# Performance work log

Hardware: AMD Instinct MI355X
Metric: run time of the kernel (lower is better)

## Reference

```python
import jax, jax.numpy as jnp
import numpy as np

AGENT, WIN = 6, 7
HEADS, DIM_HEAD = 8, 32
SCALE = DIM_HEAD ** -0.5
N = AGENT * WIN * WIN  # 294 tokens per window


def _rel_pos_index():
    # static Swin-3D relative position index, computed once in numpy
    coords = np.stack(np.meshgrid(np.arange(AGENT), np.arange(WIN), np.arange(WIN), indexing='ij'))
    flat = coords.reshape(3, -1)                      # [3, N]
    rel = flat[:, :, None] - flat[:, None, :]        # [3, N, N]
    rel = rel.transpose(1, 2, 0).copy()              # [N, N, 3]
    rel[..., 0] += AGENT - 1
    rel[..., 1] += WIN - 1
    rel[..., 2] += WIN - 1
    rel[..., 0] *= (2 * WIN - 1) * (2 * WIN - 1)
    rel[..., 1] *= 2 * WIN - 1
    return jnp.asarray(rel.sum(-1))                  # [N, N] int

RPI = _rel_pos_index()


def setup_inputs() -> dict:
    key = jax.random.key(0)
    k1, k2, k3, k4 = jax.random.split(key, 4)
    dim = 256
    x = jax.random.normal(k1, (1, AGENT, 16, 16, WIN, WIN, dim), dtype=jnp.float32)
    w_qkv = jax.random.normal(k2, (3 * HEADS * DIM_HEAD, dim), dtype=jnp.float32) * 0.02
    w_out = jax.random.normal(k3, (dim, HEADS * DIM_HEAD), dtype=jnp.float32) * 0.02
    n_bias = (2 * AGENT - 1) * (2 * WIN - 1) * (2 * WIN - 1)  # 1859
    bias_table = jax.random.normal(k4, (n_bias, HEADS), dtype=jnp.float32) * 0.02
    return {"x": x, "w_qkv": w_qkv, "w_out": w_out, "bias_table": bias_table}


def reference(x, w_qkv, w_out, bias_table):
    b, l, hx, wy, w1, w2, d = x.shape
    # 'b l x y w1 w2 d -> (b x y) (l w1 w2) d'
    xw = jnp.transpose(x, (0, 2, 3, 1, 4, 5, 6)).reshape(b * hx * wy, l * w1 * w2, d)
    qkv = xw @ w_qkv.T                                # [B, N, 3*h*dh]
    q, k, v = jnp.split(qkv, 3, axis=-1)
    def heads(t):
        B, n, _ = t.shape
        return t.reshape(B, n, HEADS, DIM_HEAD).transpose(0, 2, 1, 3)  # [B, h, N, dh]
    q, k, v = heads(q) * SCALE, heads(k), heads(v)
    sim = jnp.einsum('bhid,bhjd->bhij', q, k)        # [B, h, N, N]
    bias = bias_table[RPI]                            # [N, N, h]
    sim = sim + jnp.transpose(bias, (2, 0, 1))[None]  # broadcast over B
    attn = jax.nn.softmax(sim, axis=-1)
    out = jnp.einsum('bhij,bhjd->bhid', attn, v)      # [B, h, N, dh]
    B = b * hx * wy
    out = out.transpose(0, 2, 1, 3).reshape(B, l, w1, w2, HEADS * DIM_HEAD)
    out = out @ w_out.T                               # [B, l, w1, w2, d]
    out = out.reshape(b, hx, wy, l, w1, w2, d)
    return jnp.transpose(out, (0, 3, 1, 2, 4, 5, 6))  # b l x y w1 w2 d
```

## Files before the change

### kernel.cpp

```cpp
#include <hip/hip_runtime.h>
#include <hip/hip_bf16.h>

typedef unsigned short u16;
typedef __bf16 bf16x8_t __attribute__((ext_vector_type(8)));
typedef __bf16 bf16x4_t __attribute__((ext_vector_type(4)));
typedef float fx4 __attribute__((ext_vector_type(4)));
typedef u16 u16x8_t __attribute__((ext_vector_type(8)));
typedef u16 u16x4_t __attribute__((ext_vector_type(4)));

#define SCALE_Q 0.17677669529663687f
#define PSTR 328

__device__ __forceinline__ u16 f2bu(float f) {
  __bf16 h = (__bf16)f;
  return __builtin_bit_cast(u16, h);
}

#define GLD16(gp, lp) __builtin_amdgcn_global_load_lds( \
    (const __attribute__((address_space(1))) void*)(gp), \
    (__attribute__((address_space(3))) void*)(lp), 16, 0, 0)

__global__ void prep_x(const float* __restrict__ x, u16* __restrict__ xw) {
  int t = blockIdx.x * 256 + threadIdx.x;
  int m = t >> 5, c8 = (t & 31) * 8;
  int b = m / 294, n = m % 294;
  int hx = b >> 4, wy = b & 15;
  int l = n / 49, rem = n % 49;
  int w1 = rem / 7, w2 = rem % 7;
  size_t xoff = (((((size_t)l * 16 + hx) * 16 + wy) * 7 + w1) * 7 + w2) * 256 + c8;
  const float4* src = (const float4*)(x + xoff);
  float4 v0 = src[0], v1 = src[1];
  u16x8_t o;
  o[0] = f2bu(v0.x); o[1] = f2bu(v0.y); o[2] = f2bu(v0.z); o[3] = f2bu(v0.w);
  o[4] = f2bu(v1.x); o[5] = f2bu(v1.y); o[6] = f2bu(v1.z); o[7] = f2bu(v1.w);
  *(u16x8_t*)(xw + (size_t)m * 256 + c8) = o;
}

__global__ void prep_w(const float* __restrict__ wqkv, const float* __restrict__ wout,
                       u16* __restrict__ bqkv, u16* __restrict__ bwout) {
  int t = blockIdx.x * 256 + threadIdx.x;
  if (t < 196608) {
    float v = wqkv[t];
    if (t < 65536) v *= SCALE_Q;
    bqkv[t] = f2bu(v);
  } else {
    int i = t - 196608;
    bwout[i] = f2bu(wout[i]);
  }
}

__global__ void prep_bias(const float* __restrict__ table, u16* __restrict__ bias_pre) {
  int t = blockIdx.x * 256 + threadIdx.x;
  int lane = t & 63;
  int rest = t >> 6;
  int ct = rest % 20; rest /= 20;
  int s = rest % 19; int h = rest / 19;
  int col = ct * 16 + (lane & 15);
  int rbase = s * 16 + ((lane >> 4) << 2);
  u16x4_t o;
#pragma unroll
  for (int r = 0; r < 4; ++r) {
    float v;
    if (col >= 294) {
      v = -1e30f;
    } else {
      int i = rbase + r; if (i > 293) i = 293;
      int l1 = i / 49, r1 = i % 49, a1 = r1 / 7, b1 = r1 % 7;
      int l2 = col / 49, r2 = col % 49, a2 = r2 / 7, b2 = r2 % 7;
      int idx = (l1 - l2 + 5) * 169 + (a1 - a2 + 6) * 13 + (b1 - b2 + 6);
      v = table[idx * 8 + h];
    }
    o[r] = f2bu(v);
  }
  *(u16x4_t*)(bias_pre + (size_t)t * 4) = o;
}

template <int EPI>
__global__ __launch_bounds__(256, 2) void gemm128(const u16* __restrict__ A,
                                                  const u16* __restrict__ Bw,
                                                  u16* __restrict__ Cb,
                                                  float* __restrict__ Cf) {
  __shared__ u16 sA[128 * 32];
  __shared__ u16 sB[128 * 32];
  const int tid = threadIdx.x, lane = tid & 63, wave = tid >> 6;
  const int wr = wave >> 1, wc = wave & 1;
  const int tm = blockIdx.x, tn = blockIdx.y;
  fx4 acc[4][4] = {};
#pragma unroll 1
  for (int kt = 0; kt < 8; ++kt) {
    __syncthreads();
#pragma unroll
    for (int rnd = 0; rnd < 2; ++rnd) {
      int o = rnd * 4096 + tid * 16;
      int row = o >> 6, cb = o & 63;
      const u16* gA = A + (size_t)(tm * 128 + row) * 256 + kt * 32 + (cb >> 1);
      const u16* gB = Bw + (size_t)(tn * 128 + row) * 256 + kt * 32 + (cb >> 1);
      GLD16(gA, (char*)sA + o);
      GLD16(gB, (char*)sB + o);
    }
    __syncthreads();
    bf16x8_t af[4], bfr[4];
#pragma unroll
    for (int i = 0; i < 4; ++i)
      af[i] = *(const bf16x8_t*)&sA[(wr * 64 + i * 16 + (lane & 15)) * 32 + (lane >> 4) * 8];
#pragma unroll
    for (int j = 0; j < 4; ++j)
      bfr[j] = *(const bf16x8_t*)&sB[(wc * 64 + j * 16 + (lane & 15)) * 32 + (lane >> 4) * 8];
#pragma unroll
    for (int i = 0; i < 4; ++i)
#pragma unroll
      for (int j = 0; j < 4; ++j)
        acc[i][j] = __builtin_amdgcn_mfma_f32_16x16x32_bf16(af[i], bfr[j], acc[i][j], 0, 0, 0);
  }
  const int r0 = tm * 128 + wr * 64, c0 = tn * 128 + wc * 64;
#pragma unroll
  for (int i = 0; i < 4; ++i) {
#pragma unroll
    for (int j = 0; j < 4; ++j) {
#pragma unroll
      for (int r = 0; r < 4; ++r) {
        int row = r0 + i * 16 + (lane >> 4) * 4 + r;
        int col = c0 + j * 16 + (lane & 15);
        float v = acc[i][j][r];
        if (EPI == 0) {
          Cb[(size_t)row * 768 + col] = f2bu(v);
        } else {
          int b = row / 294, n = row % 294;
          int hx = b >> 4, wy = b & 15;
          int l = n / 49, rem = n % 49, w1 = rem / 7, w2 = rem % 7;
          size_t off = (((((size_t)l * 16 + hx) * 16 + wy) * 7 + w1) * 7 + w2) * 256 + col;
          Cf[off] = v;
        }
      }
    }
  }
}

__global__ __launch_bounds__(256, 2) void attn(const u16* __restrict__ qkv,
                                               const u16* __restrict__ bias_pre,
                                               u16* __restrict__ aout) {
  __shared__ u16 VT[32 * PSTR];
  __shared__ u16 P[4][16 * PSTR];
  const int blk = blockIdx.x;
  const int b = blk >> 3, h = blk & 7;
  const int tid = threadIdx.x, lane = tid & 63, wave = tid >> 6;
  const size_t base = (size_t)b * 294 * 768;

  for (int i = tid; i < 320 * 4; i += 256) {
    int tok = i >> 2, c8 = (i & 3) * 8;
    if (tok < 294) {
      u16x8_t v = *(const u16x8_t*)(qkv + base + (size_t)tok * 768 + 512 + h * 32 + c8);
#pragma unroll
      for (int j = 0; j < 8; ++j) VT[(c8 + j) * PSTR + tok] = v[j];
    } else {
#pragma unroll
      for (int j = 0; j < 8; ++j) VT[(c8 + j) * PSTR + tok] = 0;
    }
  }
  __syncthreads();

  u16* Pw = P[wave];
  for (int s = wave; s < 19; s += 4) {
    int qr = s * 16 + (lane & 15); if (qr > 293) qr = 293;
    bf16x8_t qf = *(const bf16x8_t*)(qkv + base + (size_t)qr * 768 + h * 32 + (lane >> 4) * 8);

    fx4 acc[20];
    const u16* bp = bias_pre + ((size_t)((h * 19 + s) * 20) * 64 + lane) * 4;
#pragma unroll
    for (int t = 0; t < 20; ++t) {
      bf16x4_t bv = *(const bf16x4_t*)(bp + t * 256);
      fx4 a; a[0] = (float)bv[0]; a[1] = (float)bv[1]; a[2] = (float)bv[2]; a[3] = (float)bv[3];
      acc[t] = a;
    }
#pragma unroll
    for (int t = 0; t < 20; ++t) {
      int kr = t * 16 + (lane & 15); if (kr > 293) kr = 293;
      bf16x8_t kf = *(const bf16x8_t*)(qkv + base + (size_t)kr * 768 + 256 + h * 32 + (lane >> 4) * 8);
      acc[t] = __builtin_amdgcn_mfma_f32_16x16x32_bf16(qf, kf, acc[t], 0, 0, 0);
    }
    float m[4], sum[4];
#pragma unroll
    for (int r = 0; r < 4; ++r) {
      float mv = acc[0][r];
#pragma unroll
      for (int t = 1; t < 20; ++t) mv = fmaxf(mv, acc[t][r]);
      mv = fmaxf(mv, __shfl_xor(mv, 1));
      mv = fmaxf(mv, __shfl_xor(mv, 2));
      mv = fmaxf(mv, __shfl_xor(mv, 4));
      mv = fmaxf(mv, __shfl_xor(mv, 8));
      m[r] = mv;
    }
#pragma unroll
    for (int r = 0; r < 4; ++r) {
      float sv = 0.f;
#pragma unroll
      for (int t = 0; t < 20; ++t) {
        float e = __expf(acc[t][r] - m[r]);
        acc[t][r] = e;
        sv += e;
      }
      sv += __shfl_xor(sv, 1);
      sv += __shfl_xor(sv, 2);
      sv += __shfl_xor(sv, 4);
      sv += __shfl_xor(sv, 8);
      sum[r] = sv;
    }
    const int prow0 = (lane >> 4) * 4;
#pragma unroll
    for (int t = 0; t < 20; ++t) {
      int pc = t * 16 + (lane & 15);
#pragma unroll
      for (int r = 0; r < 4; ++r) Pw[(prow0 + r) * PSTR + pc] = f2bu(acc[t][r]);
    }
    fx4 o0 = {}, o1 = {};
#pragma unroll
    for (int kt = 0; kt < 10; ++kt) {
      bf16x8_t pf = *(const bf16x8_t*)&Pw[(lane & 15) * PSTR + kt * 32 + (lane >> 4) * 8];
      bf16x8_t v0 = *(const bf16x8_t*)&VT[(lane & 15) * PSTR + kt * 32 + (lane >> 4) * 8];
      bf16x8_t v1 = *(const bf16x8_t*)&VT[(16 + (lane & 15)) * PSTR + kt * 32 + (lane >> 4) * 8];
      o0 = __builtin_amdgcn_mfma_f32_16x16x32_bf16(pf, v0, o0, 0, 0, 0);
      o1 = __builtin_amdgcn_mfma_f32_16x16x32_bf16(pf, v1, o1, 0, 0, 0);
    }
#pragma unroll
    for (int r = 0; r < 4; ++r) {
      int n = s * 16 + prow0 + r;
      if (n < 294) {
        float inv = 1.0f / sum[r];
        size_t ro = ((size_t)b * 294 + n) * 256 + h * 32;
        aout[ro + (lane & 15)] = f2bu(o0[r] * inv);
        aout[ro + 16 + (lane & 15)] = f2bu(o1[r] * inv);
      }
    }
  }
}

extern "C" void kernel_launch(void* const* d_in, const int* in_sizes, int n_in,
                              void* d_out, int out_size, void* d_ws, size_t ws_size,
                              hipStream_t stream) {
  (void)in_sizes; (void)n_in; (void)out_size; (void)ws_size;
  const float* x    = (const float*)d_in[0];
  const float* wqkv = (const float*)d_in[1];
  const float* wout = (const float*)d_in[2];
  const float* btab = (const float*)d_in[3];
  float* out = (float*)d_out;
  char* ws = (char*)d_ws;
  u16* xw    = (u16*)(ws);
  u16* bqkv  = (u16*)(ws + 38535168);
  u16* bwout = (u16*)(ws + 38928384);
  u16* biasp = (u16*)(ws + 39059456);
  u16* qkv   = (u16*)(ws + 40615936);
  u16* aout  = xw;

  prep_x<<<9408, 256, 0, stream>>>(x, xw);
  prep_w<<<1024, 256, 0, stream>>>(wqkv, wout, bqkv, bwout);
  prep_bias<<<760, 256, 0, stream>>>(btab, biasp);
  gemm128<0><<<dim3(588, 6), 256, 0, stream>>>(xw, bqkv, qkv, nullptr);
  attn<<<2048, 256, 0, stream>>>(qkv, biasp, aout);
  gemm128<1><<<dim3(588, 2), 256, 0, stream>>>(aout, bwout, nullptr, out);
}
```

Before: 330.0 us.

## Use 32x32 MFMA transposed S tiles, keep P in registers via permlane swap

Rewrites the attention kernel to use 32x32x16 MFMAs and computes S transposed (keys x queries), so each lane holds one query column and softmax reduces mostly in-lane with a single cross-half shuffle. The probabilities stay in registers and are rearranged into the PV operand layout with permlane32_swap, which removes the per-wave P shared-memory round trip. V^T moves to a swizzled LDS layout to cut bank conflicts. The bias precompute is reorganised to match the new 32x32 tile layout, which pads the query tiles to 320. The risks are higher register pressure (fx16 acc[10] plus packed P) and the extra padding work.

```diff
diff --git a/kernel.cpp b/kernel.cpp
--- a/kernel.cpp
+++ b/kernel.cpp
@@ -2,18 +2,26 @@
 #include <hip/hip_bf16.h>
 
 typedef unsigned short u16;
+typedef unsigned int u32;
 typedef __bf16 bf16x8_t __attribute__((ext_vector_type(8)));
-typedef __bf16 bf16x4_t __attribute__((ext_vector_type(4)));
 typedef float fx4 __attribute__((ext_vector_type(4)));
+typedef float fx16 __attribute__((ext_vector_type(16)));
 typedef u16 u16x8_t __attribute__((ext_vector_type(8)));
-typedef u16 u16x4_t __attribute__((ext_vector_type(4)));
+typedef u32 u32x2_t __attribute__((ext_vector_type(2)));
+typedef u32 u32x4_t __attribute__((ext_vector_type(4)));
 
 #define SCALE_Q 0.17677669529663687f
-#define PSTR 328
 
 __device__ __forceinline__ u16 f2bu(float f) {
   __bf16 h = (__bf16)f;
   return __builtin_bit_cast(u16, h);
+}
+__device__ __forceinline__ float bu2f(u16 b) {
+  return __builtin_bit_cast(float, (u32)b << 16);
+}
+__device__ __forceinline__ void plswap(u32& a, u32& b) {
+  u32x2_t r = __builtin_amdgcn_permlane32_swap(a, b, false, false);
+  a = r[0]; b = r[1];
 }
 
 #define GLD16(gp, lp) __builtin_amdgcn_global_load_lds( \
@@ -53,26 +61,27 @@
   int t = blockIdx.x * 256 + threadIdx.x;
   int lane = t & 63;
   int rest = t >> 6;
-  int ct = rest % 20; rest /= 20;
-  int s = rest % 19; int h = rest / 19;
-  int col = ct * 16 + (lane & 15);
-  int rbase = s * 16 + ((lane >> 4) << 2);
-  u16x4_t o;
-#pragma unroll
-  for (int r = 0; r < 4; ++r) {
+  int tile = rest % 10; rest /= 10;
+  int s = rest % 10; int h = rest / 10;
+  int q = s * 32 + (lane & 31); if (q > 293) q = 293;
+  int l1 = q / 49, r1 = q % 49, a1 = r1 / 7, b1 = r1 % 7;
+  u16x8_t o0, o1;
+#pragma unroll
+  for (int r = 0; r < 16; ++r) {
+    int key = tile * 32 + (r & 3) + 8 * (r >> 2) + 4 * (lane >> 5);
     float v;
-    if (col >= 294) {
+    if (key >= 294) {
       v = -1e30f;
     } else {
-      int i = rbase + r; if (i > 293) i = 293;
-      int l1 = i / 49, r1 = i % 49, a1 = r1 / 7, b1 = r1 % 7;
-      int l2 = col / 49, r2 = col % 49, a2 = r2 / 7, b2 = r2 % 7;
+      int l2 = key / 49, r2 = key % 49, a2 = r2 / 7, b2 = r2 % 7;
       int idx = (l1 - l2 + 5) * 169 + (a1 - a2 + 6) * 13 + (b1 - b2 + 6);
       v = table[idx * 8 + h];
     }
-    o[r] = f2bu(v);
-  }
-  *(u16x4_t*)(bias_pre + (size_t)t * 4) = o;
+    if (r < 8) o0[r] = f2bu(v); else o1[r - 8] = f2bu(v);
+  }
+  u16* dst = bias_pre + (size_t)t * 16;
+  *(u16x8_t*)(dst) = o0;
+  *(u16x8_t*)(dst + 8) = o1;
 }
 
 template <int EPI>
@@ -136,99 +145,106 @@
   }
 }
 
+__device__ __forceinline__ int vt_byte(int d, int tok) {
+  return d * 656 + ((d >> 3) & 3) * 32 + tok * 2;
+}
+
 __global__ __launch_bounds__(256, 2) void attn(const u16* __restrict__ qkv,
                                                const u16* __restrict__ bias_pre,
                                                u16* __restrict__ aout) {
-  __shared__ u16 VT[32 * PSTR];
-  __shared__ u16 P[4][16 * PSTR];
+  __shared__ __align__(16) u16 VT[10560];
   const int blk = blockIdx.x;
   const int b = blk >> 3, h = blk & 7;
   const int tid = threadIdx.x, lane = tid & 63, wave = tid >> 6;
+  const int l31 = lane & 31, g5 = lane >> 5;
   const size_t base = (size_t)b * 294 * 768;
 
-  for (int i = tid; i < 320 * 4; i += 256) {
+  for (int i = tid; i < 1280; i += 256) {
     int tok = i >> 2, c8 = (i & 3) * 8;
+    u16x8_t v;
     if (tok < 294) {
-      u16x8_t v = *(const u16x8_t*)(qkv + base + (size_t)tok * 768 + 512 + h * 32 + c8);
-#pragma unroll
-      for (int j = 0; j < 8; ++j) VT[(c8 + j) * PSTR + tok] = v[j];
+      v = *(const u16x8_t*)(qkv + base + (size_t)tok * 768 + 512 + h * 32 + c8);
     } else {
 #pragma unroll
-      for (int j = 0; j < 8; ++j) VT[(c8 + j) * PSTR + tok] = 0;
-    }
+      for (int j = 0; j < 8; ++j) v[j] = 0;
+    }
+#pragma unroll
+    for (int j = 0; j < 8; ++j)
+      *(u16*)((char*)VT + vt_byte(c8 + j, tok)) = v[j];
   }
   __syncthreads();
 
-  u16* Pw = P[wave];
-  for (int s = wave; s < 19; s += 4) {
-    int qr = s * 16 + (lane & 15); if (qr > 293) qr = 293;
-    bf16x8_t qf = *(const bf16x8_t*)(qkv + base + (size_t)qr * 768 + h * 32 + (lane >> 4) * 8);
-
-    fx4 acc[20];
-    const u16* bp = bias_pre + ((size_t)((h * 19 + s) * 20) * 64 + lane) * 4;
-#pragma unroll
-    for (int t = 0; t < 20; ++t) {
-      bf16x4_t bv = *(const bf16x4_t*)(bp + t * 256);
-      fx4 a; a[0] = (float)bv[0]; a[1] = (float)bv[1]; a[2] = (float)bv[2]; a[3] = (float)bv[3];
+#pragma unroll 1
+  for (int s = wave; s < 10; s += 4) {
+    int qr = s * 32 + l31; if (qr > 293) qr = 293;
+    const u16* qb = qkv + base + (size_t)qr * 768 + h * 32 + g5 * 8;
+    bf16x8_t qf0 = *(const bf16x8_t*)(qb);
+    bf16x8_t qf1 = *(const bf16x8_t*)(qb + 16);
+
+    fx16 acc[10];
+    const u16* bp = bias_pre + ((size_t)((h * 10 + s) * 10) * 64 + lane) * 16;
+#pragma unroll
+    for (int t = 0; t < 10; ++t) {
+      u16x8_t b0 = *(const u16x8_t*)(bp + t * 1024);
+      u16x8_t b1 = *(const u16x8_t*)(bp + t * 1024 + 8);
+      fx16 a;
+#pragma unroll
+      for (int j = 0; j < 8; ++j) { a[j] = bu2f(b0[j]); a[8 + j] = bu2f(b1[j]); }
+      int kr = t * 32 + l31; if (kr > 293) kr = 293;
+      const u16* kb = qkv + base + (size_t)kr * 768 + 256 + h * 32 + g5 * 8;
+      bf16x8_t kf0 = *(const bf16x8_t*)(kb);
+      bf16x8_t kf1 = *(const bf16x8_t*)(kb + 16);
+      a = __builtin_amdgcn_mfma_f32_32x32x16_bf16(kf0, qf0, a, 0, 0, 0);
+      a = __builtin_amdgcn_mfma_f32_32x32x16_bf16(kf1, qf1, a, 0, 0, 0);
       acc[t] = a;
     }
-#pragma unroll
-    for (int t = 0; t < 20; ++t) {
-      int kr = t * 16 + (lane & 15); if (kr > 293) kr = 293;
-      bf16x8_t kf = *(const bf16x8_t*)(qkv + base + (size_t)kr * 768 + 256 + h * 32 + (lane >> 4) * 8);
-      acc[t] = __builtin_amdgcn_mfma_f32_16x16x32_bf16(qf, kf, acc[t], 0, 0, 0);
-    }
-    float m[4], sum[4];
-#pragma unroll
-    for (int r = 0; r < 4; ++r) {
-      float mv = acc[0][r];
-#pragma unroll
-      for (int t = 1; t < 20; ++t) mv = fmaxf(mv, acc[t][r]);
-      mv = fmaxf(mv, __shfl_xor(mv, 1));
-      mv = fmaxf(mv, __shfl_xor(mv, 2));
-      mv = fmaxf(mv, __shfl_xor(mv, 4));
-      mv = fmaxf(mv, __shfl_xor(mv, 8));
-      m[r] = mv;
-    }
-#pragma unroll
-    for (int r = 0; r < 4; ++r) {
-      float sv = 0.f;
-#pragma unroll
-      for (int t = 0; t < 20; ++t) {
-        float e = __expf(acc[t][r] - m[r]);
-        acc[t][r] = e;
-        sv += e;
+
+    float mv = acc[0][0];
+#pragma unroll
+    for (int t = 0; t < 10; ++t)
+#pragma unroll
+      for (int r = 0; r < 16; ++r) mv = fmaxf(mv, acc[t][r]);
+    mv = fmaxf(mv, __shfl_xor(mv, 32));
+
+    float sv = 0.f;
+    u32 pk[10][8];
+#pragma unroll
+    for (int t = 0; t < 10; ++t) {
+      float e[16];
+#pragma unroll
+      for (int r = 0; r < 16; ++r) { e[r] = __expf(acc[t][r] - mv); sv += e[r]; }
+#pragma unroll
+      for (int j = 0; j < 8; ++j)
+        pk[t][j] = (u32)f2bu(e[2 * j]) | ((u32)f2bu(e[2 * j + 1]) << 16);
+    }
+    sv += __shfl_xor(sv, 32);
+    float inv = 1.0f / sv;
+
+    fx16 O;
+#pragma unroll
+    for (int r = 0; r < 16; ++r) O[r] = 0.f;
+#pragma unroll
+    for (int t = 0; t < 10; ++t) {
+#pragma unroll
+      for (int kh = 0; kh < 2; ++kh) {
+        u32 w0 = pk[t][kh * 4 + 0], w1 = pk[t][kh * 4 + 1];
+        u32 w2 = pk[t][kh * 4 + 2], w3 = pk[t][kh * 4 + 3];
+        plswap(w0, w2);
+        plswap(w1, w3);
+        u32x4_t w; w[0] = w0; w[1] = w1; w[2] = w2; w[3] = w3;
+        bf16x8_t pf = __builtin_bit_cast(bf16x8_t, w);
+        bf16x8_t vf = *(const bf16x8_t*)((char*)VT + vt_byte(l31, t * 32 + kh * 16 + g5 * 8));
+        O = __builtin_amdgcn_mfma_f32_32x32x16_bf16(pf, vf, O, 0, 0, 0);
       }
-      sv += __shfl_xor(sv, 1);
-      sv += __shfl_xor(sv, 2);
-      sv += __shfl_xor(sv, 4);
-      sv += __shfl_xor(sv, 8);
-      sum[r] = sv;
-    }
-    const int prow0 = (lane >> 4) * 4;
-#pragma unroll
-    for (int t = 0; t < 20; ++t) {
-      int pc = t * 16 + (lane & 15);
-#pragma unroll
-      for (int r = 0; r < 4; ++r) Pw[(prow0 + r) * PSTR + pc] = f2bu(acc[t][r]);
-    }
-    fx4 o0 = {}, o1 = {};
-#pragma unroll
-    for (int kt = 0; kt < 10; ++kt) {
-      bf16x8_t pf = *(const bf16x8_t*)&Pw[(lane & 15) * PSTR + kt * 32 + (lane >> 4) * 8];
-      bf16x8_t v0 = *(const bf16x8_t*)&VT[(lane & 15) * PSTR + kt * 32 + (lane >> 4) * 8];
-      bf16x8_t v1 = *(const bf16x8_t*)&VT[(16 + (lane & 15)) * PSTR + kt * 32 + (lane >> 4) * 8];
-      o0 = __builtin_amdgcn_mfma_f32_16x16x32_bf16(pf, v0, o0, 0, 0, 0);
-      o1 = __builtin_amdgcn_mfma_f32_16x16x32_bf16(pf, v1, o1, 0, 0, 0);
-    }
-#pragma unroll
-    for (int r = 0; r < 4; ++r) {
-      int n = s * 16 + prow0 + r;
-      if (n < 294) {
-        float inv = 1.0f / sum[r];
-        size_t ro = ((size_t)b * 294 + n) * 256 + h * 32;
-        aout[ro + (lane & 15)] = f2bu(o0[r] * inv);
-        aout[ro + 16 + (lane & 15)] = f2bu(o1[r] * inv);
+    }
+
+#pragma unroll
+    for (int r = 0; r < 16; ++r) {
+      int qrow = (r & 3) + 8 * (r >> 2) + 4 * g5;
+      int qo = s * 32 + qrow;
+      if (qo < 294) {
+        float iv = __shfl(inv, qrow);
+        aout[((size_t)b * 294 + qo) * 256 + h * 32 + l31] = f2bu(O[r] * iv);
       }
     }
   }
@@ -248,12 +264,12 @@
   u16* bqkv  = (u16*)(ws + 38535168);
   u16* bwout = (u16*)(ws + 38928384);
   u16* biasp = (u16*)(ws + 39059456);
-  u16* qkv   = (u16*)(ws + 40615936);
+  u16* qkv   = (u16*)(ws + 40697856);
   u16* aout  = xw;
 
   prep_x<<<9408, 256, 0, stream>>>(x, xw);
   prep_w<<<1024, 256, 0, stream>>>(wqkv, wout, bqkv, bwout);
-  prep_bias<<<760, 256, 0, stream>>>(btab, biasp);
+  prep_bias<<<200, 256, 0, stream>>>(btab, biasp);
   gemm128<0><<<dim3(588, 6), 256, 0, stream>>>(xw, bqkv, qkv, nullptr);
   attn<<<2048, 256, 0, stream>>>(qkv, biasp, aout);
   gemm128<1><<<dim3(588, 2), 256, 0, stream>>>(aout, bwout, nullptr, out);
```

Result: slower. 443.1 us (+34.3%).
